# Kernel optimization log

Hardware: AMD Instinct MI355X
Metric: run time of the kernel (lower is better)

The kernel has to match this reference:

```python
import jax, jax.numpy as jnp
import numpy as np

N_NODES = 50000
N_EDGES = 800000
IN_DIM = 128
HID_DIM = 128
N_GRAPHS = 512


def setup_inputs() -> dict:
    key = jax.random.key(0)
    ks = jax.random.split(key, 8)
    x = jax.random.normal(ks[0], (N_NODES, IN_DIM), dtype=jnp.float32)
    edge_index = jax.random.randint(ks[1], (2, N_EDGES), 0, N_NODES, dtype=jnp.int64)
    batch = jnp.sort(jax.random.randint(ks[2], (N_NODES,), 0, N_GRAPHS, dtype=jnp.int64))
    x_source = jax.random.randint(ks[3], (N_NODES,), 0, 2, dtype=jnp.int64)
    s1 = 1.0 / np.sqrt(IN_DIM)
    s2 = 1.0 / np.sqrt(HID_DIM)
    W1 = jax.random.normal(ks[4], (IN_DIM, HID_DIM), dtype=jnp.float32) * s1
    b1 = jnp.zeros((HID_DIM,), dtype=jnp.float32)
    W2 = jax.random.normal(ks[5], (HID_DIM, HID_DIM), dtype=jnp.float32) * s2
    b2 = jnp.zeros((HID_DIM,), dtype=jnp.float32)
    Wh = jax.random.normal(ks[6], (HID_DIM + IN_DIM, 2), dtype=jnp.float32) * (1.0 / np.sqrt(HID_DIM + IN_DIM))
    bh = jnp.zeros((2,), dtype=jnp.float32)
    return {"x": x, "edge_index": edge_index, "batch": batch, "x_source": x_source,
            "W1": W1, "b1": b1, "W2": W2, "b2": b2, "Wh": Wh, "bh": bh}


def _gcn_conv(x, W, b, src, dst, deg_inv_sqrt):
    # PyG GCNConv: h = x W; out[i] = sum_{j->i} norm_ij h[j] + norm_ii h[i] + b
    # with self-loops and symmetric normalization norm_ij = d_i^{-1/2} d_j^{-1/2}
    h = x @ W                                        # [N, out]
    norm_e = deg_inv_sqrt[src] * deg_inv_sqrt[dst]    # [E]
    msg = h[src] * norm_e[:, None]                    # gather + scale
    agg = jax.ops.segment_sum(msg, dst, num_segments=x.shape[0])
    agg = agg + h * (deg_inv_sqrt ** 2)[:, None]      # self-loop term
    return agg + b


def _mean_pool(x, seg, num_segments):
    sums = jax.ops.segment_sum(x, seg, num_segments=num_segments)
    cnt = jax.ops.segment_sum(jnp.ones((x.shape[0],), x.dtype), seg, num_segments=num_segments)
    return sums / jnp.maximum(cnt, 1.0)[:, None]


def reference(x, edge_index, batch, x_source, W1, b1, W2, b2, Wh, bh):
    src, dst = edge_index[0], edge_index[1]
    # degree with self-loops (edge weights = 1)
    deg = jax.ops.segment_sum(jnp.ones((src.shape[0],), x.dtype), dst,
                              num_segments=x.shape[0]) + 1.0
    deg_inv_sqrt = jax.lax.rsqrt(deg)

    h = jax.nn.relu(_gcn_conv(x, W1, b1, src, dst, deg_inv_sqrt))
    # dropout is identity in eval mode
    h = jax.nn.relu(_gcn_conv(h, W2, b2, src, dst, deg_inv_sqrt))

    gnn_emb = _mean_pool(h, batch, N_GRAPHS)          # [G, hid]

    # CodeBERT pooling: masked mean of raw node features where x_source == 1
    mask = (x_source == 1).astype(x.dtype)            # [N]
    summed = jax.ops.segment_sum(x * mask[:, None], batch, num_segments=N_GRAPHS)
    counts = jnp.maximum(jax.ops.segment_sum(mask, batch, num_segments=N_GRAPHS), 1.0)
    codebert_emb = summed / counts[:, None]           # [G, in]

    emb = jnp.concatenate([gnn_emb, codebert_emb], axis=1)  # [G, hid+in]
    return emb @ Wh + bh                              # [G, 2]
```

## Files before the change

kernel.cpp:

```cpp
#include <hip/hip_runtime.h>
#include <hip/hip_fp16.h>

#define NNODES 50000
#define NEDGES 800000
#define DIM    128
#define NGRAPH 512
#define NSLAB  3125
#define EPB    1024
#define NBLK_E 782
#define NBUCK  196
#define HSTRIDE NBLK_E
#define NHIST  (NBUCK * HSTRIDE)
#define NSB1   ((NHIST + 255) / 256)

typedef _Float16 f16x8 __attribute__((ext_vector_type(8)));
typedef float    f32x4 __attribute__((ext_vector_type(4)));
union U4H8 { uint4 u; f16x8 h; };

__global__ void __launch_bounds__(256) bucket_hist(const int* __restrict__ dst,
                                                   int* __restrict__ hist,
                                                   const float* __restrict__ W1,
                                                   const float* __restrict__ W2,
                                                   __half* __restrict__ Wt1,
                                                   __half* __restrict__ Wt2) {
    int t = threadIdx.x;
    if (blockIdx.x >= NBLK_E) {
        int i = (blockIdx.x - NBLK_E) * 256 + t;
        const float* W = (i < 2048) ? W1 : W2;
        __half* Wt = (i < 2048) ? Wt1 : Wt2;
        int j = i & 2047;
        int c  = j >> 4;
        int k0 = (j & 15) * 8;
        __half tmp[8];
        #pragma unroll
        for (int u = 0; u < 8; ++u) tmp[u] = (__half)W[(size_t)(k0 + u) * DIM + c];
        *(uint4*)(Wt + (size_t)c * DIM + k0) = *(uint4*)tmp;
        return;
    }
    __shared__ int cnt[NBUCK];
    if (t < NBUCK) cnt[t] = 0;
    __syncthreads();
    int e0 = blockIdx.x * EPB + t * 4;
    if (e0 + 3 < NEDGES) {
        int4 d = *(const int4*)(dst + e0);
        atomicAdd(&cnt[d.x >> 8], 1);
        atomicAdd(&cnt[d.y >> 8], 1);
        atomicAdd(&cnt[d.z >> 8], 1);
        atomicAdd(&cnt[d.w >> 8], 1);
    }
    __syncthreads();
    if (t < NBUCK) hist[t * HSTRIDE + blockIdx.x] = cnt[t];
}

__global__ void sb1(int* __restrict__ hist, int* __restrict__ partials) {
    __shared__ int s[256];
    int t = threadIdx.x;
    int gid = blockIdx.x * 256 + t;
    int v = (gid < NHIST) ? hist[gid] : 0;
    s[t] = v;
    __syncthreads();
    #pragma unroll
    for (int o = 1; o < 256; o <<= 1) {
        int u = (t >= o) ? s[t - o] : 0;
        __syncthreads();
        s[t] += u;
        __syncthreads();
    }
    if (gid < NHIST) hist[gid] = s[t] - v;
    if (t == 255) partials[blockIdx.x] = s[255];
}

__global__ void sb2(int* __restrict__ partials) {
    __shared__ int s[1024];
    int t = threadIdx.x;
    int v = (t < NSB1) ? partials[t] : 0;
    s[t] = v;
    __syncthreads();
    #pragma unroll
    for (int o = 1; o < 1024; o <<= 1) {
        int u = (t >= o) ? s[t - o] : 0;
        __syncthreads();
        s[t] += u;
        __syncthreads();
    }
    if (t < NSB1) partials[t] = s[t] - v;
}

__global__ void sb3(int* __restrict__ hist, const int* __restrict__ partials) {
    int gid = blockIdx.x * 256 + threadIdx.x;
    if (gid < NHIST) hist[gid] += partials[blockIdx.x];
}

__global__ void __launch_bounds__(256) bucket_scatter(const int* __restrict__ src,
                                                      const int* __restrict__ dst,
                                                      const int* __restrict__ hist,
                                                      unsigned* __restrict__ ebuf) {
    __shared__ int cnt[NBUCK];
    __shared__ int base[NBUCK];
    int t = threadIdx.x;
    if (t < NBUCK) { cnt[t] = 0; base[t] = hist[t * HSTRIDE + blockIdx.x]; }
    __syncthreads();
    int e0 = blockIdx.x * EPB + t * 4;
    if (e0 + 3 < NEDGES) {
        int4 s = *(const int4*)(src + e0);
        int4 d = *(const int4*)(dst + e0);
        int b, r;
        b = d.x >> 8; r = atomicAdd(&cnt[b], 1); ebuf[base[b] + r] = (unsigned)s.x | ((unsigned)(d.x & 255) << 16);
        b = d.y >> 8; r = atomicAdd(&cnt[b], 1); ebuf[base[b] + r] = (unsigned)s.y | ((unsigned)(d.y & 255) << 16);
        b = d.z >> 8; r = atomicAdd(&cnt[b], 1); ebuf[base[b] + r] = (unsigned)s.z | ((unsigned)(d.z & 255) << 16);
        b = d.w >> 8; r = atomicAdd(&cnt[b], 1); ebuf[base[b] + r] = (unsigned)s.w | ((unsigned)(d.w & 255) << 16);
    }
}

__global__ void __launch_bounds__(256) node_sort(const unsigned* __restrict__ ebuf,
                                                 const int* __restrict__ hist,
                                                 int* __restrict__ rowstart,
                                                 float* __restrict__ dis,
                                                 int* __restrict__ csr_src) {
    __shared__ int cnt[256], cnt2[256], off[256], s[256];
    int b = blockIdx.x;
    int t = threadIdx.x;
    int start = hist[b * HSTRIDE];
    int end = (b + 1 < NBUCK) ? hist[(b + 1) * HSTRIDE] : NEDGES;
    cnt[t] = 0; cnt2[t] = 0;
    __syncthreads();
    for (int i = start + t; i < end; i += 256)
        atomicAdd(&cnt[(ebuf[i] >> 16) & 255], 1);
    __syncthreads();
    s[t] = cnt[t];
    __syncthreads();
    #pragma unroll
    for (int o = 1; o < 256; o <<= 1) {
        int u = (t >= o) ? s[t - o] : 0;
        __syncthreads();
        s[t] += u;
        __syncthreads();
    }
    off[t] = s[t] - cnt[t];
    int node = b * 256 + t;
    if (node < NNODES) {
        rowstart[node] = start + off[t];
        dis[node] = rsqrtf((float)cnt[t] + 1.0f);
    }
    if (b == NBUCK - 1 && t == 0) rowstart[NNODES] = NEDGES;
    __syncthreads();
    for (int i = start + t; i < end; i += 256) {
        unsigned e = ebuf[i];
        int j = (e >> 16) & 255;
        int r = atomicAdd(&cnt2[j], 1);
        csr_src[start + off[j] + r] = (int)(e & 0xFFFFu);
    }
}

template<typename XT>
__global__ void __launch_bounds__(256) gemm_mfma(const XT* __restrict__ X,
                                                 const __half* __restrict__ Wt,
                                                 const float* __restrict__ dis,
                                                 __half* __restrict__ Y) {
    __shared__ __align__(16) unsigned char Wl[128 * 256];

    const int t = threadIdx.x;
    {
        int col = t >> 1;
        int kb0 = (t & 1) * 128;
        const unsigned char* g = (const unsigned char*)Wt + col * 256 + kb0;
        #pragma unroll
        for (int i = 0; i < 8; ++i) {
            uint4 v = *(const uint4*)(g + i * 16);
            int kb = kb0 + i * 16;
            *(uint4*)(Wl + col * 256 + (kb ^ ((col & 7) << 4))) = v;
        }
    }
    __syncthreads();

    int wave = t >> 6;
    int slab = blockIdx.x * 4 + wave;
    if (slab >= NSLAB) return;
    int l  = t & 63;
    int lr = l & 15;
    int lg = l >> 4;

    int arow = slab * 16 + lr;

    f16x8 afr[4];
    if constexpr (sizeof(XT) == 4) {
        const float* xr = (const float*)X + (size_t)arow * DIM;
        #pragma unroll
        for (int c = 0; c < 4; ++c) {
            int k0 = c * 32 + lg * 8;
            float4 u0 = *(const float4*)(xr + k0);
            float4 u1 = *(const float4*)(xr + k0 + 4);
            f16x8 a;
            a[0] = (_Float16)u0.x; a[1] = (_Float16)u0.y;
            a[2] = (_Float16)u0.z; a[3] = (_Float16)u0.w;
            a[4] = (_Float16)u1.x; a[5] = (_Float16)u1.y;
            a[6] = (_Float16)u1.z; a[7] = (_Float16)u1.w;
            afr[c] = a;
        }
    } else {
        const __half* xr = (const __half*)X + (size_t)arow * DIM;
        #pragma unroll
        for (int c = 0; c < 4; ++c) {
            U4H8 u; u.u = *(const uint4*)(xr + c * 32 + lg * 8);
            afr[c] = u.h;
        }
    }

    f32x4 acc[8];
    #pragma unroll
    for (int jt = 0; jt < 8; ++jt) acc[jt] = (f32x4){0.f, 0.f, 0.f, 0.f};

    #pragma unroll
    for (int c = 0; c < 4; ++c) {
        #pragma unroll
        for (int jt = 0; jt < 8; ++jt) {
            int col = jt * 16 + lr;
            int kb  = c * 64 + lg * 16;
            U4H8 bb;
            bb.u = *(const uint4*)(Wl + col * 256 + (kb ^ ((col & 7) << 4)));
            acc[jt] = __builtin_amdgcn_mfma_f32_16x16x32_f16(afr[c], bb.h, acc[jt], 0, 0, 0);
        }
    }

    float4 dv = *(const float4*)(dis + slab * 16 + lg * 4);
    float dsc[4] = {dv.x, dv.y, dv.z, dv.w};
    #pragma unroll
    for (int j = 0; j < 4; ++j) {
        int row = slab * 16 + lg * 4 + j;
        __half* yr = Y + (size_t)row * DIM + lr;
        #pragma unroll
        for (int jt = 0; jt < 8; ++jt)
            yr[jt * 16] = (__half)(acc[jt][j] * dsc[j]);
    }
}

__device__ __forceinline__ void acc_add(float4& a, uint2 u) {
    float2 f0 = __half22float2(*(__half2*)&u.x);
    float2 f1 = __half22float2(*(__half2*)&u.y);
    a.x += f0.x; a.y += f0.y; a.z += f1.x; a.w += f1.y;
}

__global__ void __launch_bounds__(256) gcn_gather(const __half* __restrict__ hwh,
                                                  const int* __restrict__ rowstart,
                                                  const int* __restrict__ csr_src,
                                                  const float* __restrict__ dis,
                                                  const float* __restrict__ b,
                                                  __half* __restrict__ outh) {
    int t = blockIdx.x * 256 + threadIdx.x;
    int d = t >> 5, q = t & 31;
    if (d >= NNODES) return;
    const uint2* hw8 = (const uint2*)hwh;

    float4 a0 = make_float4(0.f, 0.f, 0.f, 0.f);
    float4 a1 = a0, a2 = a0, a3 = a0, a4 = a0, a5 = a0, a6 = a0, a7 = a0;

    acc_add(a0, hw8[(size_t)d * 32 + q]);

    int beg = rowstart[d], end = rowstart[d + 1];
    int i = beg;
    for (; i + 8 <= end; i += 8) {
        int s0 = csr_src[i + 0], s1 = csr_src[i + 1];
        int s2 = csr_src[i + 2], s3 = csr_src[i + 3];
        int s4 = csr_src[i + 4], s5 = csr_src[i + 5];
        int s6 = csr_src[i + 6], s7 = csr_src[i + 7];
        uint2 v0 = hw8[(size_t)s0 * 32 + q];
        uint2 v1 = hw8[(size_t)s1 * 32 + q];
        uint2 v2 = hw8[(size_t)s2 * 32 + q];
        uint2 v3 = hw8[(size_t)s3 * 32 + q];
        uint2 v4 = hw8[(size_t)s4 * 32 + q];
        uint2 v5 = hw8[(size_t)s5 * 32 + q];
        uint2 v6 = hw8[(size_t)s6 * 32 + q];
        uint2 v7 = hw8[(size_t)s7 * 32 + q];
        acc_add(a0, v0); acc_add(a1, v1); acc_add(a2, v2); acc_add(a3, v3);
        acc_add(a4, v4); acc_add(a5, v5); acc_add(a6, v6); acc_add(a7, v7);
    }
    for (; i + 2 <= end; i += 2) {
        uint2 v0 = hw8[(size_t)csr_src[i + 0] * 32 + q];
        uint2 v1 = hw8[(size_t)csr_src[i + 1] * 32 + q];
        acc_add(a0, v0); acc_add(a1, v1);
    }
    if (i < end) acc_add(a0, hw8[(size_t)csr_src[i] * 32 + q]);

    a0.x += a1.x + a2.x + a3.x + a4.x + a5.x + a6.x + a7.x;
    a0.y += a1.y + a2.y + a3.y + a4.y + a5.y + a6.y + a7.y;
    a0.z += a1.z + a2.z + a3.z + a4.z + a5.z + a6.z + a7.z;
    a0.w += a1.w + a2.w + a3.w + a4.w + a5.w + a6.w + a7.w;

    float dd = dis[d];
    float4 bb = ((const float4*)b)[q];
    __half ot[4];
    ot[0] = (__half)fmaxf(fmaf(a0.x, dd, bb.x), 0.f);
    ot[1] = (__half)fmaxf(fmaf(a0.y, dd, bb.y), 0.f);
    ot[2] = (__half)fmaxf(fmaf(a0.z, dd, bb.z), 0.f);
    ot[3] = (__half)fmaxf(fmaf(a0.w, dd, bb.w), 0.f);
    ((uint2*)outh)[(size_t)d * 32 + q] = *(uint2*)ot;
}

__device__ __forceinline__ int lower_bound_i(const int* __restrict__ a, int n, int v) {
    int lo = 0, hi = n;
    while (lo < hi) {
        int mid = (lo + hi) >> 1;
        if (a[mid] < v) lo = mid + 1; else hi = mid;
    }
    return lo;
}

__global__ void __launch_bounds__(256) pool_head(const __half* __restrict__ h,
                                                 const float* __restrict__ x,
                                                 const int* __restrict__ batch,
                                                 const int* __restrict__ xsrc,
                                                 const float* __restrict__ Wh,
                                                 const float* __restrict__ bh,
                                                 float* __restrict__ out) {
    __shared__ float sAG[DIM];
    __shared__ float sAC[DIM];
    __shared__ int   sSC;
    int g   = blockIdx.x;
    int t   = threadIdx.x;
    int sub = t >> 5;
    int q   = t & 31;

    if (t < DIM) { sAG[t] = 0.f; sAC[t] = 0.f; }
    if (t == 0) sSC = 0;
    __syncthreads();

    int lo = lower_bound_i(batch, NNODES, g);
    int hi = lower_bound_i(batch, NNODES, g + 1);

    float4 ag = make_float4(0.f, 0.f, 0.f, 0.f);
    float4 ac = make_float4(0.f, 0.f, 0.f, 0.f);
    int sc = 0;
    const uint2* h8 = (const uint2*)h;
    const float4* x4 = (const float4*)x;
    for (int r = lo + sub; r < hi; r += 8) {
        acc_add(ag, h8[(size_t)r * 32 + q]);
        if (xsrc[r] == 1) {
            float4 xv = x4[(size_t)r * 32 + q];
            ac.x += xv.x; ac.y += xv.y; ac.z += xv.z; ac.w += xv.w;
            sc++;
        }
    }
    float* agp = sAG + q * 4;
    atomicAdd(agp + 0, ag.x); atomicAdd(agp + 1, ag.y);
    atomicAdd(agp + 2, ag.z); atomicAdd(agp + 3, ag.w);
    float* acp = sAC + q * 4;
    atomicAdd(acp + 0, ac.x); atomicAdd(acp + 1, ac.y);
    atomicAdd(acp + 2, ac.z); atomicAdd(acp + 3, ac.w);
    if (q == 0 && sc) atomicAdd(&sSC, sc);
    __syncthreads();

    if (t < 32) {
        float invg = 1.0f / fmaxf((float)(hi - lo), 1.0f);
        float invc = 1.0f / fmaxf((float)sSC, 1.0f);
        const float2* Wh2 = (const float2*)Wh;
        float a0 = 0.f, a1 = 0.f;
        #pragma unroll
        for (int j = 0; j < 4; ++j) {
            float e1 = sAG[t * 4 + j] * invg;
            float2 w1 = Wh2[t * 4 + j];
            a0 = fmaf(e1, w1.x, a0);
            a1 = fmaf(e1, w1.y, a1);
            float e2 = sAC[t * 4 + j] * invc;
            float2 w2 = Wh2[DIM + t * 4 + j];
            a0 = fmaf(e2, w2.x, a0);
            a1 = fmaf(e2, w2.y, a1);
        }
        #pragma unroll
        for (int off = 16; off; off >>= 1) {
            a0 += __shfl_down(a0, off, 32);
            a1 += __shfl_down(a1, off, 32);
        }
        if (t == 0) {
            out[g * 2 + 0] = a0 + bh[0];
            out[g * 2 + 1] = a1 + bh[1];
        }
    }
}

extern "C" void kernel_launch(void* const* d_in, const int* in_sizes, int n_in,
                              void* d_out, int out_size, void* d_ws, size_t ws_size,
                              hipStream_t stream) {
    const float* x     = (const float*)d_in[0];
    const int*   ei    = (const int*)d_in[1];
    const int*   batch = (const int*)d_in[2];
    const int*   xsrc  = (const int*)d_in[3];
    const float* W1 = (const float*)d_in[4];
    const float* b1 = (const float*)d_in[5];
    const float* W2 = (const float*)d_in[6];
    const float* b2 = (const float*)d_in[7];
    const float* Wh = (const float*)d_in[8];
    const float* bh = (const float*)d_in[9];
    float* out = (float*)d_out;

    const int* src = ei;
    const int* dst = ei + NEDGES;

    float* ws = (float*)d_ws;
    size_t off = 0;
    float*    dis      = ws + off;              off += 50048;
    int*      rowstart = (int*)(ws + off);      off += 50048;
    int*      hist     = (int*)(ws + off);      off += ((NHIST + 255) & ~255);
    int*      partials = (int*)(ws + off);      off += 1024;
    unsigned* ebuf     = (unsigned*)(ws + off); off += 800000;
    int*      csr_src  = (int*)(ws + off);      off += 800000;
    __half*   Wt1      = (__half*)(ws + off);   off += 8192;
    __half*   Wt2      = (__half*)(ws + off);   off += 8192;
    __half*   hwh      = (__half*)(ws + off);   off += (size_t)NNODES * DIM / 2;
    __half*   hbuf     = (__half*)(ws + off);   off += (size_t)NNODES * DIM / 2;

    bucket_hist<<<NBLK_E + 16, 256, 0, stream>>>(dst, hist, W1, W2, Wt1, Wt2);
    sb1<<<NSB1, 256, 0, stream>>>(hist, partials);
    sb2<<<1, 1024, 0, stream>>>(partials);
    sb3<<<NSB1, 256, 0, stream>>>(hist, partials);
    bucket_scatter<<<NBLK_E, 256, 0, stream>>>(src, dst, hist, ebuf);
    node_sort<<<NBUCK, 256, 0, stream>>>(ebuf, hist, rowstart, dis, csr_src);

    const int ngemm = (NSLAB + 3) / 4;

    gemm_mfma<float><<<ngemm, 256, 0, stream>>>(x, Wt1, dis, hwh);
    gcn_gather<<<(NNODES * 32) / 256, 256, 0, stream>>>(hwh, rowstart, csr_src, dis, b1, hbuf);

    gemm_mfma<__half><<<ngemm, 256, 0, stream>>>(hbuf, Wt2, dis, hwh);
    gcn_gather<<<(NNODES * 32) / 256, 256, 0, stream>>>(hwh, rowstart, csr_src, dis, b2, hbuf);

    pool_head<<<NGRAPH, 256, 0, stream>>>(hbuf, x, batch, xsrc, Wh, bh, out);
}
```

Before: 148.0 us.

## Replace three-kernel global scan with per-bucket scan and redundant base scan

Replaces the three-pass global exclusive scan over the bucket histogram with one kernel that scans each bucket's row of block counts and emits per-bucket totals. The scatter and node-sort kernels each recompute the small exclusive scan over the 196 bucket totals in shared memory. This removes two kernel launches and a dependent serial pass. In exchange, every block in scatter and node_sort does extra redundant scan work and synchronization.

After: 145.7 us. Within noise of the previous version (-1.6%).

```diff
diff --git a/kernel.cpp b/kernel.cpp
--- a/kernel.cpp
+++ b/kernel.cpp
@@ -11,7 +11,6 @@
 #define NBUCK  196
 #define HSTRIDE NBLK_E
 #define NHIST  (NBUCK * HSTRIDE)
-#define NSB1   ((NHIST + 255) / 256)
 
 typedef _Float16 f16x8 __attribute__((ext_vector_type(8)));
 typedef float    f32x4 __attribute__((ext_vector_type(4)));
@@ -52,12 +51,21 @@
     if (t < NBUCK) hist[t * HSTRIDE + blockIdx.x] = cnt[t];
 }
 
-__global__ void sb1(int* __restrict__ hist, int* __restrict__ partials) {
+__global__ void __launch_bounds__(256) scan1(int* __restrict__ hist, int* __restrict__ btot) {
     __shared__ int s[256];
+    int b = blockIdx.x;
     int t = threadIdx.x;
-    int gid = blockIdx.x * 256 + t;
-    int v = (gid < NHIST) ? hist[gid] : 0;
-    s[t] = v;
+    int* hb = hist + b * HSTRIDE;
+    int i0 = t * 4;
+    int v[4];
+    int loc = 0;
+    #pragma unroll
+    for (int u = 0; u < 4; ++u) {
+        int idx = i0 + u;
+        v[u] = (idx < HSTRIDE) ? hb[idx] : 0;
+        loc += v[u];
+    }
+    s[t] = loc;
     __syncthreads();
     #pragma unroll
     for (int o = 1; o < 256; o <<= 1) {
@@ -66,62 +74,70 @@
         s[t] += u;
         __syncthreads();
     }
-    if (gid < NHIST) hist[gid] = s[t] - v;
-    if (t == 255) partials[blockIdx.x] = s[255];
-}
-
-__global__ void sb2(int* __restrict__ partials) {
-    __shared__ int s[1024];
-    int t = threadIdx.x;
-    int v = (t < NSB1) ? partials[t] : 0;
+    int run = s[t] - loc;
+    #pragma unroll
+    for (int u = 0; u < 4; ++u) {
+        int idx = i0 + u;
+        if (idx < HSTRIDE) hb[idx] = run;
+        run += v[u];
+    }
+    if (t == 255) btot[b] = run;
+}
+
+__device__ __forceinline__ void base_scan(const int* __restrict__ btot, int* __restrict__ bex,
+                                          int* __restrict__ s, int t) {
+    int v = (t < NBUCK) ? btot[t] : 0;
     s[t] = v;
     __syncthreads();
     #pragma unroll
-    for (int o = 1; o < 1024; o <<= 1) {
+    for (int o = 1; o < 256; o <<= 1) {
         int u = (t >= o) ? s[t - o] : 0;
         __syncthreads();
         s[t] += u;
         __syncthreads();
     }
-    if (t < NSB1) partials[t] = s[t] - v;
-}
-
-__global__ void sb3(int* __restrict__ hist, const int* __restrict__ partials) {
-    int gid = blockIdx.x * 256 + threadIdx.x;
-    if (gid < NHIST) hist[gid] += partials[blockIdx.x];
+    if (t < NBUCK) bex[t] = s[t] - v;
+    if (t == 0) bex[NBUCK] = NEDGES;
+    __syncthreads();
 }
 
 __global__ void __launch_bounds__(256) bucket_scatter(const int* __restrict__ src,
                                                       const int* __restrict__ dst,
                                                       const int* __restrict__ hist,
+                                                      const int* __restrict__ btot,
                                                       unsigned* __restrict__ ebuf) {
     __shared__ int cnt[NBUCK];
-    __shared__ int base[NBUCK];
+    __shared__ int sbase[NBUCK];
+    __shared__ int bex[NBUCK + 1];
+    __shared__ int s[256];
     int t = threadIdx.x;
-    if (t < NBUCK) { cnt[t] = 0; base[t] = hist[t * HSTRIDE + blockIdx.x]; }
+    base_scan(btot, bex, s, t);
+    if (t < NBUCK) { cnt[t] = 0; sbase[t] = bex[t] + hist[t * HSTRIDE + blockIdx.x]; }
     __syncthreads();
     int e0 = blockIdx.x * EPB + t * 4;
     if (e0 + 3 < NEDGES) {
-        int4 s = *(const int4*)(src + e0);
+        int4 sv = *(const int4*)(src + e0);
         int4 d = *(const int4*)(dst + e0);
         int b, r;
-        b = d.x >> 8; r = atomicAdd(&cnt[b], 1); ebuf[base[b] + r] = (unsigned)s.x | ((unsigned)(d.x & 255) << 16);
-        b = d.y >> 8; r = atomicAdd(&cnt[b], 1); ebuf[base[b] + r] = (unsigned)s.y | ((unsigned)(d.y & 255) << 16);
-        b = d.z >> 8; r = atomicAdd(&cnt[b], 1); ebuf[base[b] + r] = (unsigned)s.z | ((unsigned)(d.z & 255) << 16);
-        b = d.w >> 8; r = atomicAdd(&cnt[b], 1); ebuf[base[b] + r] = (unsigned)s.w | ((unsigned)(d.w & 255) << 16);
+        b = d.x >> 8; r = atomicAdd(&cnt[b], 1); ebuf[sbase[b] + r] = (unsigned)sv.x | ((unsigned)(d.x & 255) << 16);
+        b = d.y >> 8; r = atomicAdd(&cnt[b], 1); ebuf[sbase[b] + r] = (unsigned)sv.y | ((unsigned)(d.y & 255) << 16);
+        b = d.z >> 8; r = atomicAdd(&cnt[b], 1); ebuf[sbase[b] + r] = (unsigned)sv.z | ((unsigned)(d.z & 255) << 16);
+        b = d.w >> 8; r = atomicAdd(&cnt[b], 1); ebuf[sbase[b] + r] = (unsigned)sv.w | ((unsigned)(d.w & 255) << 16);
     }
 }
 
 __global__ void __launch_bounds__(256) node_sort(const unsigned* __restrict__ ebuf,
-                                                 const int* __restrict__ hist,
+                                                 const int* __restrict__ btot,
                                                  int* __restrict__ rowstart,
                                                  float* __restrict__ dis,
                                                  int* __restrict__ csr_src) {
     __shared__ int cnt[256], cnt2[256], off[256], s[256];
+    __shared__ int bex[NBUCK + 1];
     int b = blockIdx.x;
     int t = threadIdx.x;
-    int start = hist[b * HSTRIDE];
-    int end = (b + 1 < NBUCK) ? hist[(b + 1) * HSTRIDE] : NEDGES;
+    base_scan(btot, bex, s, t);
+    int start = bex[b];
+    int end   = bex[b + 1];
     cnt[t] = 0; cnt2[t] = 0;
     __syncthreads();
     for (int i = start + t; i < end; i += 256)
@@ -400,7 +416,7 @@
     float*    dis      = ws + off;              off += 50048;
     int*      rowstart = (int*)(ws + off);      off += 50048;
     int*      hist     = (int*)(ws + off);      off += ((NHIST + 255) & ~255);
-    int*      partials = (int*)(ws + off);      off += 1024;
+    int*      btot     = (int*)(ws + off);      off += 256;
     unsigned* ebuf     = (unsigned*)(ws + off); off += 800000;
     int*      csr_src  = (int*)(ws + off);      off += 800000;
     __half*   Wt1      = (__half*)(ws + off);   off += 8192;
@@ -409,11 +425,9 @@
     __half*   hbuf     = (__half*)(ws + off);   off += (size_t)NNODES * DIM / 2;
 
     bucket_hist<<<NBLK_E + 16, 256, 0, stream>>>(dst, hist, W1, W2, Wt1, Wt2);
-    sb1<<<NSB1, 256, 0, stream>>>(hist, partials);
-    sb2<<<1, 1024, 0, stream>>>(partials);
-    sb3<<<NSB1, 256, 0, stream>>>(hist, partials);
-    bucket_scatter<<<NBLK_E, 256, 0, stream>>>(src, dst, hist, ebuf);
-    node_sort<<<NBUCK, 256, 0, stream>>>(ebuf, hist, rowstart, dis, csr_src);
+    scan1<<<NBUCK, 256, 0, stream>>>(hist, btot);
+    bucket_scatter<<<NBLK_E, 256, 0, stream>>>(src, dst, hist, btot, ebuf);
+    node_sort<<<NBUCK, 256, 0, stream>>>(ebuf, btot, rowstart, dis, csr_src);
 
     const int ngemm = (NSLAB + 3) / 4;
 
```
